# Optimization experiments

Hardware: AMD Instinct MI355X
Metric: run time of the kernel (lower is better)

## Reference

```python
import jax, jax.numpy as jnp
import numpy as np

H, W = 64, 64
DELTA = 5.0
EPS = 1e-8
ITERS = 3
LN_EPS = 1e-5


def _make_grid():
    # abs_grid in [-1, 1], shape (H, W, 2) -- matches S_p init range
    ys = jnp.linspace(-1.0, 1.0, H)
    xs = jnp.linspace(-1.0, 1.0, W)
    gy, gx = jnp.meshgrid(ys, xs, indexing='ij')
    return jnp.stack([gy, gx], axis=-1).astype(jnp.float32)


def _ln(x, g, b):
    m = jnp.mean(x, -1, keepdims=True)
    v = jnp.mean((x - m) ** 2, -1, keepdims=True)
    return (x - m) * jax.lax.rsqrt(v + LN_EPS) * g + b


def _mlp2(x, w1, b1, w2, b2):
    return jax.nn.relu(x @ w1.T + b1) @ w2.T + b2


def _gru(x, h, wih, whh, bih, bhh):
    gi = x @ wih.T + bih
    gh = h @ whh.T + bhh
    ir, iz, inn = jnp.split(gi, 3, -1)
    hr, hz, hn = jnp.split(gh, 3, -1)
    r = jax.nn.sigmoid(ir + hr)
    z = jax.nn.sigmoid(iz + hz)
    nn_ = jnp.tanh(inn + r * hn)
    return (1.0 - z) * nn_ + z * h


def setup_inputs() -> dict:
    key = jax.random.key(0)
    ks = jax.random.split(key, 30)
    b, n_s, d, hd = 8, 8, 128, 128
    n = H * W
    s = 0.02
    inp = {}
    inp['inputs'] = jax.random.normal(ks[0], (b, n, d), jnp.float32)
    inp['slots_init'] = jax.random.normal(ks[1], (b, n_s, d), jnp.float32)
    inp['S_p0'] = 2.0 * jax.random.uniform(ks[2], (b, n_s, 2), jnp.float32) - 1.0
    inp['S_s'] = 0.01 * jax.random.normal(ks[3], (b, n_s, 2), jnp.float32) + 0.1
    inp['S_r'] = (np.pi / 4.0) * jnp.tanh(jax.random.normal(ks[4], (b, n_s, 2, 2), jnp.float32))
    inp['Wq'] = s * jax.random.normal(ks[5], (d, d), jnp.float32)
    inp['Wk'] = s * jax.random.normal(ks[6], (d, d), jnp.float32)
    inp['Wv'] = s * jax.random.normal(ks[7], (d, d), jnp.float32)
    inp['g_w'] = s * jax.random.normal(ks[8], (d, 2), jnp.float32)
    inp['g_b'] = s * jax.random.normal(ks[9], (d,), jnp.float32)
    inp['f_w1'] = s * jax.random.normal(ks[10], (hd, d), jnp.float32)
    inp['f_b1'] = s * jax.random.normal(ks[11], (hd,), jnp.float32)
    inp['f_w2'] = s * jax.random.normal(ks[12], (d, hd), jnp.float32)
    inp['f_b2'] = s * jax.random.normal(ks[13], (d,), jnp.float32)
    inp['gru_wih'] = s * jax.random.normal(ks[14], (3 * d, d), jnp.float32)
    inp['gru_whh'] = s * jax.random.normal(ks[15], (3 * d, d), jnp.float32)
    inp['gru_bih'] = s * jax.random.normal(ks[16], (3 * d,), jnp.float32)
    inp['gru_bhh'] = s * jax.random.normal(ks[17], (3 * d,), jnp.float32)
    inp['mlp_w1'] = s * jax.random.normal(ks[18], (hd, d), jnp.float32)
    inp['mlp_b1'] = s * jax.random.normal(ks[19], (hd,), jnp.float32)
    inp['mlp_w2'] = s * jax.random.normal(ks[20], (d, hd), jnp.float32)
    inp['mlp_b2'] = s * jax.random.normal(ks[21], (d,), jnp.float32)
    inp['ln_s_g'] = jnp.ones((d,), jnp.float32)
    inp['ln_s_b'] = jnp.zeros((d,), jnp.float32)
    inp['ln_pf_g'] = jnp.ones((d,), jnp.float32)
    inp['ln_pf_b'] = jnp.zeros((d,), jnp.float32)
    return inp


def reference(inputs, slots_init, S_p0, S_s, S_r, Wq, Wk, Wv, g_w, g_b,
              f_w1, f_b1, f_w2, f_b2, gru_wih, gru_whh, gru_bih, gru_bhh,
              mlp_w1, mlp_b1, mlp_w2, mlp_b2, ln_s_g, ln_s_b, ln_pf_g, ln_pf_b):
    b, n, d = inputs.shape
    n_s = slots_init.shape[1]
    scale = d ** -0.5
    grid = _make_grid()            # (H, W, 2)
    grid_flat = grid.reshape(n, 2)  # (HW, 2)

    to_k = (inputs @ Wk.T)[:, None]  # (b, 1, n, d)
    to_v = (inputs @ Wv.T)[:, None]

    slots = slots_init
    S_p = S_p0
    for _ in range(ITERS):
        slots_prev = slots
        slots_n = _ln(slots, ln_s_g, ln_s_b)
        # per-slot relative grid: (b, n_s, H, W, 2)
        rel = (grid[None, None] - S_p[:, :, None, None, :]) / DELTA
        pos = (rel @ g_w.T + g_b).reshape(b, n_s, n, d)  # (b, n_s, HW, d)
        k = _mlp2(to_k + pos, f_w1, f_b1, f_w2, f_b2)     # (b, n_s, HW, d)
        v = _mlp2(to_v + pos, f_w1, f_b1, f_w2, f_b2)
        q = slots_n @ Wq.T                                # (b, n_s, d)
        dots = jnp.einsum('bid,bijd->bij', q, k) * scale  # (b, n_s, HW)
        attn = jax.nn.softmax(dots, axis=1) + EPS          # softmax over slots
        attn = attn / jnp.sum(attn, -1, keepdims=True)
        updates = jnp.einsum('bijd,bij->bid', v, attn)    # (b, n_s, d)
        # per-slot attention-weighted centroid (vectorized over slots)
        S_p = jnp.einsum('bij,jc->bic', attn, grid_flat) / jnp.sum(attn, -1, keepdims=True)
        slots = _gru(updates.reshape(-1, d), slots_prev.reshape(-1, d),
                     gru_wih, gru_whh, gru_bih, gru_bhh).reshape(b, n_s, d)
        slots = slots + _mlp2(_ln(slots, ln_pf_g, ln_pf_b), mlp_w1, mlp_b1, mlp_w2, mlp_b2)
    return slots, S_p, S_r, S_s
```

## Files before the change

kernel.cpp:

```cpp
#include <hip/hip_runtime.h>
#include <cstdint>
#include <cstddef>

#define SCALE  0.08838834764831845f
#define EPS_   1e-8f
#define LN_EPS_ 1e-5f

typedef unsigned short ushort_t;
typedef unsigned int uint_t;
typedef __attribute__((ext_vector_type(8))) short short8;
typedef __attribute__((ext_vector_type(4))) float f32x4;

constexpr int OFF_GFD   = 0;
constexpr int OFF_CB    = 256;
constexpr int OFF_QB    = 384;
constexpr int OFF_SP    = 448;
constexpr int OFF_OQ    = 576;
constexpr int OFF_SLOTS = 16960;
constexpr int OFF_ZP    = 25152;
constexpr int OFF_PP    = 29248;
constexpr int OFF_UP    = 37440;
constexpr int OFF_WKB   = 561728;
constexpr int OFF_WVB   = 569920;
constexpr int OFF_FW2T  = 578112;
constexpr int OFF_BKT   = 594496;
constexpr int OFF_BV    = 2691648;
constexpr int OFF_AB    = 4788800;

__device__ __forceinline__ float waveReduceSum(float v) {
#pragma unroll
  for (int m = 1; m < 64; m <<= 1) v += __shfl_xor(v, m, 64);
  return v;
}
__device__ __forceinline__ float bf2f(uint_t u) { return __uint_as_float(u << 16); }
__device__ __forceinline__ ushort_t f2bf(float f) {
  uint_t u = __float_as_uint(f);
  return (ushort_t)((u + 0x7fffu + ((u >> 16) & 1u)) >> 16);
}

__device__ __forceinline__ float halfDot(const float* __restrict__ Wrow,
                                         const float* xv, int h) {
  const float4* wr = (const float4*)Wrow + h * 16;
  const float4* xr = (const float4*)xv + h * 16;
  float4 a = {0.f, 0.f, 0.f, 0.f};
#pragma unroll
  for (int i = 0; i < 16; ++i) {
    float4 wv = wr[i], xq = xr[i];
    a.x = fmaf(wv.x, xq.x, a.x);
    a.y = fmaf(wv.y, xq.y, a.y);
    a.z = fmaf(wv.z, xq.z, a.z);
    a.w = fmaf(wv.w, xq.w, a.w);
  }
  return (a.x + a.y) + (a.z + a.w);
}

__device__ __forceinline__ float quarterDot(const float* __restrict__ Wrow,
                                            const float* xv, int h) {
  const float4* wr = (const float4*)Wrow + h * 8;
  const float4* xr = (const float4*)xv + h * 8;
  float4 a = {0.f, 0.f, 0.f, 0.f};
#pragma unroll
  for (int i = 0; i < 8; ++i) {
    float4 wv = wr[i], xq = xr[i];
    a.x = fmaf(wv.x, xq.x, a.x);
    a.y = fmaf(wv.y, xq.y, a.y);
    a.z = fmaf(wv.z, xq.z, a.z);
    a.w = fmaf(wv.w, xq.w, a.w);
  }
  return (a.x + a.y) + (a.z + a.w);
}
__device__ __forceinline__ float quadSum(float v) {
  v += __shfl_xor(v, 1, 64);
  v += __shfl_xor(v, 2, 64);
  return v;
}

__global__ __launch_bounds__(256) void kFold(
    const float* __restrict__ f_w1, const float* __restrict__ Wk,
    const float* __restrict__ Wv, const float* __restrict__ g_w,
    const float* __restrict__ g_b, const float* __restrict__ f_b1,
    const float* __restrict__ f_w2, const float* __restrict__ slots_init,
    const float* __restrict__ S_p0, const float* __restrict__ inputs,
    float* __restrict__ ws) {
  int blk = blockIdx.x, tid = threadIdx.x;
  if (blk < 128) {
    int isV = blk >> 6;
    int idx = (blk & 63) * 256 + tid;
    int h = idx >> 7, e = idx & 127;
    const float* Wm = isV ? Wv : Wk;
    float a = 0.f;
#pragma unroll 4
    for (int d = 0; d < 128; ++d) a = fmaf(f_w1[h * 128 + d], Wm[d * 128 + e], a);
    ((ushort_t*)(ws + (isV ? OFF_WVB : OFF_WKB)))[idx] = f2bf(a);
  } else if (blk == 128) {
    int h = tid >> 1, c = tid & 1;
    float a = 0.f;
    for (int d = 0; d < 128; ++d) a = fmaf(f_w1[h * 128 + d], g_w[d * 2 + c], a);
    ws[OFF_GFD + tid] = a * 0.2f;
  } else if (blk == 129) {
    if (tid < 128) {
      float a = f_b1[tid];
      for (int d = 0; d < 128; ++d) a = fmaf(f_w1[tid * 128 + d], g_b[d], a);
      ws[OFF_CB + tid] = a;
    }
  } else if (blk == 130) {
    for (int i = tid; i < 16384; i += 256)
      ws[OFF_FW2T + (i & 127) * 128 + (i >> 7)] = f_w2[i];
  } else if (blk < 135) {
    int base = (blk - 131) * 2048 + tid * 8;
    float4 a = *(const float4*)&slots_init[base];
    float4 b = *(const float4*)&slots_init[base + 4];
    *(float4*)&ws[OFF_SLOTS + base] = a;
    *(float4*)&ws[OFF_SLOTS + base + 4] = b;
  } else if (blk == 135) {
    if (tid < 128) ws[OFF_SP + tid] = S_p0[tid];
  } else {
    int idx = (blk - 136) * 256 + tid;
    const float4* src = (const float4*)(inputs + (size_t)idx * 8);
    float4 a = src[0], b = src[1];
    uint_t p0 = (uint_t)f2bf(a.x) | ((uint_t)f2bf(a.y) << 16);
    uint_t p1 = (uint_t)f2bf(a.z) | ((uint_t)f2bf(a.w) << 16);
    uint_t p2 = (uint_t)f2bf(b.x) | ((uint_t)f2bf(b.y) << 16);
    uint_t p3 = (uint_t)f2bf(b.z) | ((uint_t)f2bf(b.w) << 16);
    ((uint4*)((ushort_t*)(ws + OFF_AB)))[idx] = make_uint4(p0, p1, p2, p3);
  }
}

struct QSm { float yl[128]; float ql[128]; float red[4]; float red2[4]; };

__device__ void doQ(int bs, const float* __restrict__ Wq,
                    const float* __restrict__ f_b2,
                    const float* __restrict__ lnsg,
                    const float* __restrict__ lnsb,
                    float* __restrict__ ws, QSm& S) {
  int t = threadIdx.x, w = t >> 6, lane = t & 63;
  int d = w * 32 + (lane >> 1), h = lane & 1;
  const float* FW2T = ws + OFF_FW2T;
  float x = ws[OFF_SLOTS + bs * 128 + d];
  float m1 = waveReduceSum(h == 0 ? x : 0.f);
  float m2 = waveReduceSum(h == 0 ? x * x : 0.f);
  if (lane == 0) { S.red[w] = m1; S.red2[w] = m2; }
  __syncthreads();
  float mean = (S.red[0] + S.red[1] + S.red[2] + S.red[3]) * (1.f / 128.f);
  float var = (S.red2[0] + S.red2[1] + S.red2[2] + S.red2[3]) * (1.f / 128.f) - mean * mean;
  if (h == 0) S.yl[d] = (x - mean) * rsqrtf(var + LN_EPS_) * lnsg[d] + lnsb[d];
  __syncthreads();
  float q = halfDot(Wq + (size_t)d * 128, S.yl, h);
  q += __shfl_xor(q, 1, 64);
  if (h == 0) S.ql[d] = q;
  __syncthreads();
  float qv = waveReduceSum(h == 0 ? q * f_b2[d] : 0.f);
  if (lane == 0) S.red[w] = qv;
  float qf = halfDot(FW2T + (size_t)d * 128, S.ql, h);
  qf += __shfl_xor(qf, 1, 64);
  __syncthreads();
  if (t == 0) ws[OFF_QB + bs] = (S.red[0] + S.red[1] + S.red[2] + S.red[3]) * SCALE;
  if (h == 0) {
    float sp0 = ws[OFF_SP + bs * 2 + 0], sp1 = ws[OFF_SP + bs * 2 + 1];
    float offd = -(sp0 * ws[OFF_GFD + d * 2 + 0] + sp1 * ws[OFF_GFD + d * 2 + 1]);
    ws[OFF_OQ + (bs * 128 + d) * 2 + 0] = offd;
    ws[OFF_OQ + (bs * 128 + d) * 2 + 1] = qf * SCALE;
  }
}

__global__ __launch_bounds__(256) void kBaseQ(const float* __restrict__ Wq,
                                              const float* __restrict__ f_b2,
                                              const float* __restrict__ lnsg,
                                              const float* __restrict__ lnsb,
                                              float* __restrict__ ws) {
  __shared__ __align__(16) char smem[17408];
  int blk = blockIdx.x;
  if (blk >= 1024) {
    doQ(blk - 1024, Wq, f_b2, lnsg, lnsb, ws, *reinterpret_cast<QSm*>(smem));
    return;
  }
  char* ep = smem;
  const ushort_t* ab = (const ushort_t*)(ws + OFF_AB);
  int tid = threadIdx.x, w = tid >> 6, l = tid & 63;
  int lr = l & 15, lg = l >> 4;
  int mat = blk >> 9;
  int rb = blk & 511;
  int b = rb >> 6;
  int n0 = (rb & 63) * 64;
  const ushort_t* Wg = (const ushort_t*)(ws + (mat ? OFF_WVB : OFF_WKB));

  short8 afrag[4];
#pragma unroll
  for (int ks = 0; ks < 4; ++ks) {
    size_t row = (size_t)b * 4096 + n0 + w * 16 + lr;
    afrag[ks] = *(const short8*)(ab + row * 128 + ks * 32 + lg * 8);
  }
  float gf0a[8], gf1a[8], cba[8];
#pragma unroll
  for (int ct = 0; ct < 8; ++ct) {
    int c = ct * 16 + lr;
    gf0a[ct] = ws[OFF_GFD + c * 2 + 0];
    gf1a[ct] = ws[OFF_GFD + c * 2 + 1];
    cba[ct]  = ws[OFF_CB + c];
  }
  f32x4 acc[8];
#pragma unroll
  for (int ct = 0; ct < 8; ++ct) acc[ct] = (f32x4){0.f, 0.f, 0.f, 0.f};
#pragma unroll 2
  for (int ct = 0; ct < 8; ++ct) {
    short8 bfr[4];
#pragma unroll
    for (int ks = 0; ks < 4; ++ks)
      bfr[ks] = *(const short8*)(Wg + (ct * 16 + lr) * 128 + ks * 32 + lg * 8);
#pragma unroll
    for (int ks = 0; ks < 4; ++ks)
      acc[ct] = __builtin_amdgcn_mfma_f32_16x16x32_bf16(afrag[ks], bfr[ks], acc[ct], 0, 0, 0);
  }
#pragma unroll
  for (int ct = 0; ct < 8; ++ct) {
    int c = ct * 16 + lr;
    ushort_t pk[4];
#pragma unroll
    for (int r = 0; r < 4; ++r) {
      int nl = w * 16 + lg * 4 + r;
      int n = n0 + nl;
      float gy = -1.f + (float)(n >> 6) * (2.f / 63.f);
      float gx = -1.f + (float)(n & 63) * (2.f / 63.f);
      float o = acc[ct][r] + gy * gf0a[ct] + gx * gf1a[ct] + cba[ct];
      pk[r] = f2bf(o);
    }
    if (mat == 0) {
      int nl0 = w * 16 + lg * 4;
      int byte = (c * 128 + nl0 * 2) ^ ((c & 7) << 4);
      *(uint2*)(ep + byte) = make_uint2(
          (uint_t)pk[0] | ((uint_t)pk[1] << 16),
          (uint_t)pk[2] | ((uint_t)pk[3] << 16));
    } else {
      int nl0 = w * 16 + lg * 4;
#pragma unroll
      for (int r = 0; r < 4; ++r)
        *(ushort_t*)(ep + (nl0 + r) * 272 + c * 2) = pk[r];
    }
  }
  __syncthreads();
  if (mat == 0) {
    uint_t* outK = (uint_t*)(ws + OFF_BKT);
    for (int idx = tid; idx < 1024; idx += 256) {
      int dp = idx >> 4, j = idx & 15;
      int c0 = 2 * dp, c1 = 2 * dp + 1;
      uint2 aA = *(const uint2*)(ep + ((c0 * 128 + j * 8) ^ ((c0 & 7) << 4)));
      uint2 bA = *(const uint2*)(ep + ((c1 * 128 + j * 8) ^ ((c1 & 7) << 4)));
      uint4 o;
      o.x = (aA.x & 0xffffu) | (bA.x << 16);
      o.y = (aA.x >> 16) | (bA.x & 0xffff0000u);
      o.z = (aA.y & 0xffffu) | (bA.y << 16);
      o.w = (aA.y >> 16) | (bA.y & 0xffff0000u);
      *(uint4*)(outK + ((size_t)(b * 64 + dp)) * 4096 + n0 + j * 4) = o;
    }
  } else {
    ushort_t* outV = (ushort_t*)(ws + OFF_BV);
    for (int idx = tid; idx < 1024; idx += 256) {
      int nl = idx >> 4, j = idx & 15;
      uint4 v = *(const uint4*)(ep + nl * 272 + j * 16);
      *(uint4*)(outV + ((size_t)rb * 64 + nl) * 128 + j * 8) = v;
    }
  }
}

__global__ __launch_bounds__(256) void kAttn(float* __restrict__ ws) {
  __shared__ __align__(16) float OFFl[8][128];
  __shared__ __align__(16) float QFl[8][128];
  __shared__ float tp[64][37];
  __shared__ __align__(16) float al[64][12];
  __shared__ float Ush[4][8][132];
  int b = blockIdx.x >> 6, chunk = blockIdx.x & 63;
  int tid = threadIdx.x, w = tid >> 6, lane = tid & 63;
  int sb = b * 8;
  for (int f = tid; f < 1024; f += 256) {
    int s = f >> 7, d = f & 127;
    float2 oq = *(const float2*)&ws[OFF_OQ + ((sb + s) * 128 + d) * 2];
    OFFl[s][d] = oq.x;
    QFl[s][d] = oq.y;
  }
  float qbl[8];
#pragma unroll
  for (int s = 0; s < 8; ++s) qbl[s] = ws[OFF_QB + sb + s];
  __syncthreads();

  int n = chunk * 64 + lane;
  const uint_t* kpp = (const uint_t*)(ws + OFF_BKT) +
                      (size_t)b * 262144 + (size_t)(w * 16) * 4096 + n;
  float t[8];
#pragma unroll
  for (int s = 0; s < 8; ++s) t[s] = 0.f;
#pragma unroll 4
  for (int dp = 0; dp < 16; ++dp) {
    uint_t v = kpp[(size_t)dp * 4096];
    float k0 = bf2f(v & 0xffffu);
    float k1 = bf2f(v >> 16);
    int d0 = w * 32 + 2 * dp;
#pragma unroll
    for (int s = 0; s < 8; ++s) {
      float2 ofp = *(const float2*)&OFFl[s][d0];
      float2 qfp = *(const float2*)&QFl[s][d0];
      t[s] = fmaf(fmaxf(k0 + ofp.x, 0.f), qfp.x, t[s]);
      t[s] = fmaf(fmaxf(k1 + ofp.y, 0.f), qfp.y, t[s]);
    }
  }
#pragma unroll
  for (int s = 0; s < 8; ++s) tp[lane][s * 4 + w] = t[s];
  __syncthreads();
  float a[8], den = 0.f;
#pragma unroll
  for (int s = 0; s < 8; ++s)
    t[s] = tp[lane][s * 4 + 0] + tp[lane][s * 4 + 1] +
           tp[lane][s * 4 + 2] + tp[lane][s * 4 + 3] + qbl[s];
  float mx = t[0];
#pragma unroll
  for (int s = 1; s < 8; ++s) mx = fmaxf(mx, t[s]);
#pragma unroll
  for (int s = 0; s < 8; ++s) { a[s] = __expf(t[s] - mx); den += a[s]; }
  float inv = 1.0f / den;
#pragma unroll
  for (int s = 0; s < 8; ++s) a[s] = fmaf(a[s], inv, EPS_);
  if (w == 0) {
    float gy = -1.f + (float)(n >> 6) * (2.f / 63.f);
    float gx = -1.f + (float)(n & 63) * (2.f / 63.f);
#pragma unroll
    for (int s = 0; s < 8; ++s) al[lane][s] = a[s];
#pragma unroll
    for (int s = 0; s < 8; ++s) {
      float z = waveReduceSum(a[s]);
      float p0 = waveReduceSum(a[s] * gy);
      float p1 = waveReduceSum(a[s] * gx);
      if (lane == 0) {
        ws[OFF_ZP + (b * 64 + chunk) * 8 + s] = z;
        ws[OFF_PP + ((b * 64 + chunk) * 8 + s) * 2 + 0] = p0;
        ws[OFF_PP + ((b * 64 + chunk) * 8 + s) * 2 + 1] = p1;
      }
    }
  }
  __syncthreads();

  int c0 = 2 * lane;
  float offv0[8], offv1[8];
#pragma unroll
  for (int s = 0; s < 8; ++s) {
    float2 of2 = *(const float2*)&OFFl[s][c0];
    offv0[s] = of2.x;
    offv1[s] = of2.y;
  }
  float Ua0[8], Ua1[8];
#pragma unroll
  for (int s = 0; s < 8; ++s) { Ua0[s] = 0.f; Ua1[s] = 0.f; }
  const ushort_t* vp = (const ushort_t*)(ws + OFF_BV) +
                       ((size_t)(b * 4096 + chunk * 64 + w * 16)) * 128 + c0;
#pragma unroll 4
  for (int i = 0; i < 16; ++i) {
    uint_t vraw = *(const uint_t*)(vp + (size_t)i * 128);
    float v0 = bf2f(vraw & 0xffffu);
    float v1 = bf2f(vraw >> 16);
    int ii = w * 16 + i;
    float4 a0 = *(const float4*)&al[ii][0];
    float4 a1 = *(const float4*)&al[ii][4];
    float asv[8] = {a0.x, a0.y, a0.z, a0.w, a1.x, a1.y, a1.z, a1.w};
#pragma unroll
    for (int s = 0; s < 8; ++s) {
      Ua0[s] = fmaf(asv[s], fmaxf(v0 + offv0[s], 0.f), Ua0[s]);
      Ua1[s] = fmaf(asv[s], fmaxf(v1 + offv1[s], 0.f), Ua1[s]);
    }
  }
#pragma unroll
  for (int s = 0; s < 8; ++s) {
    Ush[w][s][c0] = Ua0[s];
    Ush[w][s][c0 + 1] = Ua1[s];
  }
  __syncthreads();
  for (int f = tid; f < 1024; f += 256) {
    int s = f >> 7, c = f & 127;
    float v = Ush[0][s][c] + Ush[1][s][c] + Ush[2][s][c] + Ush[3][s][c];
    ws[OFF_UP + ((size_t)(b * 64 + chunk) * 8 + s) * 128 + c] = v;
  }
}

__global__ __launch_bounds__(512) void kCQ(
    const float* __restrict__ Wq, const float* __restrict__ f_w2,
    const float* __restrict__ f_b2, const float* __restrict__ wih,
    const float* __restrict__ whh, const float* __restrict__ bih,
    const float* __restrict__ bhh, const float* __restrict__ mw1,
    const float* __restrict__ mb1, const float* __restrict__ mw2,
    const float* __restrict__ mb2, const float* __restrict__ lnpg,
    const float* __restrict__ lnpb, const float* __restrict__ lnsg,
    const float* __restrict__ lnsb, const float* __restrict__ S_r,
    const float* __restrict__ S_s, float* __restrict__ ws,
    float* __restrict__ out, int last) {
  int bs = blockIdx.x;
  int t = threadIdx.x;
  if (bs == 64) {
    if (t < 256) out[8320 + t] = S_r[t];
    else if (t < 384) out[8576 + t - 256] = S_s[t - 256];
    return;
  }
  int b = bs >> 3, s = bs & 7;
  int w = t >> 6, lane = t & 63;
  int d = t >> 2, h = t & 3;
  __shared__ __align__(16) float ul[128], xl[128], sl[128], yl[128], hml[128];
  __shared__ float red[8], red2[8];
  const float* FW2T = ws + OFF_FW2T;
  float zv = ws[OFF_ZP + (b * 64 + lane) * 8 + s];
  float2 pv = *(const float2*)&ws[OFF_PP + ((size_t)(b * 64 + lane) * 8 + s) * 2];
  float Z = waveReduceSum(zv);
  float P0 = waveReduceSum(pv.x);
  float P1 = waveReduceSum(pv.y);
  float invZ = 1.f / Z, sp0 = P0 * invZ, sp1 = P1 * invZ;
  float u = 0.f;
  const float* up = ws + OFF_UP + ((size_t)(b * 64 + h * 16) * 8 + s) * 128 + d;
#pragma unroll
  for (int ch = 0; ch < 16; ++ch) u += up[(size_t)ch * 1024];
  u = quadSum(u);
  if (h == 0) { ul[d] = u * invZ; sl[d] = ws[OFF_SLOTS + bs * 128 + d]; }
  if (t == 0) {
    ws[OFF_SP + bs * 2 + 0] = sp0;
    ws[OFF_SP + bs * 2 + 1] = sp1;
    if (last) {
      out[8192 + bs * 2 + 0] = sp0;
      out[8192 + bs * 2 + 1] = sp1;
    }
  }
  __syncthreads();
  float xa = quadSum(quarterDot(f_w2 + (size_t)d * 128, ul, h));
  if (h == 0) xl[d] = xa + f_b2[d];
  __syncthreads();
  float ir = quarterDot(wih + (size_t)d * 128, xl, h);
  float iz = quarterDot(wih + (size_t)(128 + d) * 128, xl, h);
  float in_ = quarterDot(wih + (size_t)(256 + d) * 128, xl, h);
  float hr = quarterDot(whh + (size_t)d * 128, sl, h);
  float hz = quarterDot(whh + (size_t)(128 + d) * 128, sl, h);
  float hn = quarterDot(whh + (size_t)(256 + d) * 128, sl, h);
  ir = quadSum(ir); iz = quadSum(iz); in_ = quadSum(in_);
  hr = quadSum(hr); hz = quadSum(hz); hn = quadSum(hn);
  float hnew = 0.f;
  if (h == 0) {
    float rg = 1.f / (1.f + __expf(-(ir + bih[d] + hr + bhh[d])));
    float zg = 1.f / (1.f + __expf(-(iz + bih[128 + d] + hz + bhh[128 + d])));
    float ng = tanhf(in_ + bih[256 + d] + rg * (hn + bhh[256 + d]));
    hnew = (1.f - zg) * ng + zg * sl[d];
  }
  float m1 = waveReduceSum(h == 0 ? hnew : 0.f);
  float m2 = waveReduceSum(h == 0 ? hnew * hnew : 0.f);
  if (lane == 0) { red[w] = m1; red2[w] = m2; }
  __syncthreads();
  float mean = 0.f, var = 0.f;
#pragma unroll
  for (int i = 0; i < 8; ++i) { mean += red[i]; var += red2[i]; }
  mean *= (1.f / 128.f);
  var = var * (1.f / 128.f) - mean * mean;
  if (h == 0) yl[d] = (hnew - mean) * rsqrtf(var + LN_EPS_) * lnpg[d] + lnpb[d];
  __syncthreads();
  float hm = quadSum(quarterDot(mw1 + (size_t)d * 128, yl, h));
  if (h == 0) hml[d] = fmaxf(hm + mb1[d], 0.f);
  __syncthreads();
  float oa = quadSum(quarterDot(mw2 + (size_t)d * 128, hml, h));
  float o = 0.f;
  if (h == 0) {
    o = hnew + mb2[d] + oa;
    ws[OFF_SLOTS + bs * 128 + d] = o;
    if (last) out[bs * 128 + d] = o;
  }
  float n1 = waveReduceSum(h == 0 ? o : 0.f);
  float n2 = waveReduceSum(h == 0 ? o * o : 0.f);
  if (lane == 0) { red[w] = n1; red2[w] = n2; }
  __syncthreads();
  float mean2 = 0.f, var2 = 0.f;
#pragma unroll
  for (int i = 0; i < 8; ++i) { mean2 += red[i]; var2 += red2[i]; }
  mean2 *= (1.f / 128.f);
  var2 = var2 * (1.f / 128.f) - mean2 * mean2;
  if (h == 0) yl[d] = (o - mean2) * rsqrtf(var2 + LN_EPS_) * lnsg[d] + lnsb[d];
  __syncthreads();
  float q = quadSum(quarterDot(Wq + (size_t)d * 128, yl, h));
  if (h == 0) xl[d] = q;
  __syncthreads();
  float qv = waveReduceSum(h == 0 ? q * f_b2[d] : 0.f);
  if (lane == 0) red[w] = qv;
  float qf = quadSum(quarterDot(FW2T + (size_t)d * 128, xl, h));
  __syncthreads();
  if (t == 0) {
    float qb = 0.f;
#pragma unroll
    for (int i = 0; i < 8; ++i) qb += red[i];
    ws[OFF_QB + bs] = qb * SCALE;
  }
  if (h == 0) {
    float offd = -(sp0 * ws[OFF_GFD + d * 2 + 0] + sp1 * ws[OFF_GFD + d * 2 + 1]);
    ws[OFF_OQ + (bs * 128 + d) * 2 + 0] = offd;
    ws[OFF_OQ + (bs * 128 + d) * 2 + 1] = qf * SCALE;
  }
}

extern "C" void kernel_launch(void* const* d_in, const int* in_sizes, int n_in,
                              void* d_out, int out_size, void* d_ws, size_t ws_size,
                              hipStream_t stream) {
  const float* inputs     = (const float*)d_in[0];
  const float* slots_init = (const float*)d_in[1];
  const float* S_p0       = (const float*)d_in[2];
  const float* S_s        = (const float*)d_in[3];
  const float* S_r        = (const float*)d_in[4];
  const float* Wq   = (const float*)d_in[5];
  const float* Wk   = (const float*)d_in[6];
  const float* Wv   = (const float*)d_in[7];
  const float* g_w  = (const float*)d_in[8];
  const float* g_b  = (const float*)d_in[9];
  const float* f_w1 = (const float*)d_in[10];
  const float* f_b1 = (const float*)d_in[11];
  const float* f_w2 = (const float*)d_in[12];
  const float* f_b2 = (const float*)d_in[13];
  const float* gwih = (const float*)d_in[14];
  const float* gwhh = (const float*)d_in[15];
  const float* gbih = (const float*)d_in[16];
  const float* gbhh = (const float*)d_in[17];
  const float* mw1  = (const float*)d_in[18];
  const float* mb1  = (const float*)d_in[19];
  const float* mw2  = (const float*)d_in[20];
  const float* mb2  = (const float*)d_in[21];
  const float* lnsg = (const float*)d_in[22];
  const float* lnsb = (const float*)d_in[23];
  const float* lnpg = (const float*)d_in[24];
  const float* lnpb = (const float*)d_in[25];
  float* ws  = (float*)d_ws;
  float* out = (float*)d_out;

  kFold<<<392, 256, 0, stream>>>(f_w1, Wk, Wv, g_w, g_b, f_b1, f_w2,
                                 slots_init, S_p0, inputs, ws);
  kBaseQ<<<1088, 256, 0, stream>>>(Wq, f_b2, lnsg, lnsb, ws);
  for (int it = 0; it < 3; ++it) {
    int last = (it == 2);
    kAttn<<<512, 256, 0, stream>>>(ws);
    kCQ<<<64 + last, 512, 0, stream>>>(Wq, f_w2, f_b2, gwih, gwhh, gbih, gbhh,
                                       mw1, mb1, mw2, mb2, lnpg, lnpb,
                                       lnsg, lnsb, S_r, S_s, ws, out, last);
  }
}
```

Measured before the change: 165.6 us.

## Fuse K/V projection with first attention pass and fold initial Q into prep kernel

```diff
diff --git a/kernel.cpp b/kernel.cpp
--- a/kernel.cpp
+++ b/kernel.cpp
@@ -81,7 +81,10 @@
     const float* __restrict__ g_b, const float* __restrict__ f_b1,
     const float* __restrict__ f_w2, const float* __restrict__ slots_init,
     const float* __restrict__ S_p0, const float* __restrict__ inputs,
-    float* __restrict__ ws) {
+    const float* __restrict__ Wq, const float* __restrict__ f_b2,
+    const float* __restrict__ lnsg, const float* __restrict__ lnsb,
+    const float* __restrict__ S_r, const float* __restrict__ S_s,
+    float* __restrict__ ws, float* __restrict__ out) {
   int blk = blockIdx.x, tid = threadIdx.x;
   if (blk < 128) {
     int isV = blk >> 6;
@@ -114,7 +117,7 @@
     *(float4*)&ws[OFF_SLOTS + base + 4] = b;
   } else if (blk == 135) {
     if (tid < 128) ws[OFF_SP + tid] = S_p0[tid];
-  } else {
+  } else if (blk < 392) {
     int idx = (blk - 136) * 256 + tid;
     const float4* src = (const float4*)(inputs + (size_t)idx * 8);
     float4 a = src[0], b = src[1];
@@ -123,159 +126,70 @@
     uint_t p2 = (uint_t)f2bf(b.x) | ((uint_t)f2bf(b.y) << 16);
     uint_t p3 = (uint_t)f2bf(b.z) | ((uint_t)f2bf(b.w) << 16);
     ((uint4*)((ushort_t*)(ws + OFF_AB)))[idx] = make_uint4(p0, p1, p2, p3);
-  }
-}
-
-struct QSm { float yl[128]; float ql[128]; float red[4]; float red2[4]; };
-
-__device__ void doQ(int bs, const float* __restrict__ Wq,
-                    const float* __restrict__ f_b2,
-                    const float* __restrict__ lnsg,
-                    const float* __restrict__ lnsb,
-                    float* __restrict__ ws, QSm& S) {
-  int t = threadIdx.x, w = t >> 6, lane = t & 63;
-  int d = w * 32 + (lane >> 1), h = lane & 1;
-  const float* FW2T = ws + OFF_FW2T;
-  float x = ws[OFF_SLOTS + bs * 128 + d];
-  float m1 = waveReduceSum(h == 0 ? x : 0.f);
-  float m2 = waveReduceSum(h == 0 ? x * x : 0.f);
-  if (lane == 0) { S.red[w] = m1; S.red2[w] = m2; }
-  __syncthreads();
-  float mean = (S.red[0] + S.red[1] + S.red[2] + S.red[3]) * (1.f / 128.f);
-  float var = (S.red2[0] + S.red2[1] + S.red2[2] + S.red2[3]) * (1.f / 128.f) - mean * mean;
-  if (h == 0) S.yl[d] = (x - mean) * rsqrtf(var + LN_EPS_) * lnsg[d] + lnsb[d];
-  __syncthreads();
-  float q = halfDot(Wq + (size_t)d * 128, S.yl, h);
-  q += __shfl_xor(q, 1, 64);
-  if (h == 0) S.ql[d] = q;
-  __syncthreads();
-  float qv = waveReduceSum(h == 0 ? q * f_b2[d] : 0.f);
-  if (lane == 0) S.red[w] = qv;
-  float qf = halfDot(FW2T + (size_t)d * 128, S.ql, h);
-  qf += __shfl_xor(qf, 1, 64);
-  __syncthreads();
-  if (t == 0) ws[OFF_QB + bs] = (S.red[0] + S.red[1] + S.red[2] + S.red[3]) * SCALE;
-  if (h == 0) {
-    float sp0 = ws[OFF_SP + bs * 2 + 0], sp1 = ws[OFF_SP + bs * 2 + 1];
-    float offd = -(sp0 * ws[OFF_GFD + d * 2 + 0] + sp1 * ws[OFF_GFD + d * 2 + 1]);
-    ws[OFF_OQ + (bs * 128 + d) * 2 + 0] = offd;
-    ws[OFF_OQ + (bs * 128 + d) * 2 + 1] = qf * SCALE;
-  }
-}
-
-__global__ __launch_bounds__(256) void kBaseQ(const float* __restrict__ Wq,
-                                              const float* __restrict__ f_b2,
-                                              const float* __restrict__ lnsg,
-                                              const float* __restrict__ lnsb,
-                                              float* __restrict__ ws) {
-  __shared__ __align__(16) char smem[17408];
-  int blk = blockIdx.x;
-  if (blk >= 1024) {
-    doQ(blk - 1024, Wq, f_b2, lnsg, lnsb, ws, *reinterpret_cast<QSm*>(smem));
-    return;
-  }
-  char* ep = smem;
-  const ushort_t* ab = (const ushort_t*)(ws + OFF_AB);
-  int tid = threadIdx.x, w = tid >> 6, l = tid & 63;
-  int lr = l & 15, lg = l >> 4;
-  int mat = blk >> 9;
-  int rb = blk & 511;
-  int b = rb >> 6;
-  int n0 = (rb & 63) * 64;
-  const ushort_t* Wg = (const ushort_t*)(ws + (mat ? OFF_WVB : OFF_WKB));
-
-  short8 afrag[4];
-#pragma unroll
-  for (int ks = 0; ks < 4; ++ks) {
-    size_t row = (size_t)b * 4096 + n0 + w * 16 + lr;
-    afrag[ks] = *(const short8*)(ab + row * 128 + ks * 32 + lg * 8);
-  }
-  float gf0a[8], gf1a[8], cba[8];
-#pragma unroll
-  for (int ct = 0; ct < 8; ++ct) {
-    int c = ct * 16 + lr;
-    gf0a[ct] = ws[OFF_GFD + c * 2 + 0];
-    gf1a[ct] = ws[OFF_GFD + c * 2 + 1];
-    cba[ct]  = ws[OFF_CB + c];
-  }
-  f32x4 acc[8];
-#pragma unroll
-  for (int ct = 0; ct < 8; ++ct) acc[ct] = (f32x4){0.f, 0.f, 0.f, 0.f};
-#pragma unroll 2
-  for (int ct = 0; ct < 8; ++ct) {
-    short8 bfr[4];
-#pragma unroll
-    for (int ks = 0; ks < 4; ++ks)
-      bfr[ks] = *(const short8*)(Wg + (ct * 16 + lr) * 128 + ks * 32 + lg * 8);
-#pragma unroll
-    for (int ks = 0; ks < 4; ++ks)
-      acc[ct] = __builtin_amdgcn_mfma_f32_16x16x32_bf16(afrag[ks], bfr[ks], acc[ct], 0, 0, 0);
-  }
-#pragma unroll
-  for (int ct = 0; ct < 8; ++ct) {
-    int c = ct * 16 + lr;
-    ushort_t pk[4];
-#pragma unroll
-    for (int r = 0; r < 4; ++r) {
-      int nl = w * 16 + lg * 4 + r;
-      int n = n0 + nl;
-      float gy = -1.f + (float)(n >> 6) * (2.f / 63.f);
-      float gx = -1.f + (float)(n & 63) * (2.f / 63.f);
-      float o = acc[ct][r] + gy * gf0a[ct] + gx * gf1a[ct] + cba[ct];
-      pk[r] = f2bf(o);
-    }
-    if (mat == 0) {
-      int nl0 = w * 16 + lg * 4;
-      int byte = (c * 128 + nl0 * 2) ^ ((c & 7) << 4);
-      *(uint2*)(ep + byte) = make_uint2(
-          (uint_t)pk[0] | ((uint_t)pk[1] << 16),
-          (uint_t)pk[2] | ((uint_t)pk[3] << 16));
-    } else {
-      int nl0 = w * 16 + lg * 4;
-#pragma unroll
-      for (int r = 0; r < 4; ++r)
-        *(ushort_t*)(ep + (nl0 + r) * 272 + c * 2) = pk[r];
-    }
-  }
-  __syncthreads();
-  if (mat == 0) {
-    uint_t* outK = (uint_t*)(ws + OFF_BKT);
-    for (int idx = tid; idx < 1024; idx += 256) {
-      int dp = idx >> 4, j = idx & 15;
-      int c0 = 2 * dp, c1 = 2 * dp + 1;
-      uint2 aA = *(const uint2*)(ep + ((c0 * 128 + j * 8) ^ ((c0 & 7) << 4)));
-      uint2 bA = *(const uint2*)(ep + ((c1 * 128 + j * 8) ^ ((c1 & 7) << 4)));
-      uint4 o;
-      o.x = (aA.x & 0xffffu) | (bA.x << 16);
-      o.y = (aA.x >> 16) | (bA.x & 0xffff0000u);
-      o.z = (aA.y & 0xffffu) | (bA.y << 16);
-      o.w = (aA.y >> 16) | (bA.y & 0xffff0000u);
-      *(uint4*)(outK + ((size_t)(b * 64 + dp)) * 4096 + n0 + j * 4) = o;
+  } else if (blk < 456) {
+    int bs = blk - 392;
+    __shared__ __align__(16) float yl[128], ql[128], gwsp[128];
+    __shared__ float red[4], red2[4];
+    int t = tid, w = t >> 6, lane = t & 63;
+    int d = w * 32 + (lane >> 1), h = lane & 1;
+    float sp0 = S_p0[bs * 2 + 0], sp1 = S_p0[bs * 2 + 1];
+    if (t < 128) gwsp[t] = sp0 * g_w[t * 2 + 0] + sp1 * g_w[t * 2 + 1];
+    float x = slots_init[bs * 128 + d];
+    float m1 = waveReduceSum(h == 0 ? x : 0.f);
+    float m2 = waveReduceSum(h == 0 ? x * x : 0.f);
+    if (lane == 0) { red[w] = m1; red2[w] = m2; }
+    __syncthreads();
+    float mean = (red[0] + red[1] + red[2] + red[3]) * (1.f / 128.f);
+    float var = (red2[0] + red2[1] + red2[2] + red2[3]) * (1.f / 128.f) - mean * mean;
+    if (h == 0) yl[d] = (x - mean) * rsqrtf(var + LN_EPS_) * lnsg[d] + lnsb[d];
+    __syncthreads();
+    float q = halfDot(Wq + (size_t)d * 128, yl, h);
+    q += __shfl_xor(q, 1, 64);
+    if (h == 0) ql[d] = q;
+    __syncthreads();
+    float qv = waveReduceSum(h == 0 ? q * f_b2[d] : 0.f);
+    if (lane == 0) red[w] = qv;
+    float qf = 0.f;
+    const float* fcol = f_w2 + (size_t)(h * 64) * 128 + d;
+#pragma unroll 4
+    for (int e = 0; e < 64; ++e) qf = fmaf(ql[h * 64 + e], fcol[(size_t)e * 128], qf);
+    qf += __shfl_xor(qf, 1, 64);
+    float od = halfDot(f_w1 + (size_t)d * 128, gwsp, h);
+    od += __shfl_xor(od, 1, 64);
+    __syncthreads();
+    if (t == 0) ws[OFF_QB + bs] = (red[0] + red[1] + red[2] + red[3]) * SCALE;
+    if (h == 0) {
+      ws[OFF_OQ + (bs * 128 + d) * 2 + 0] = -0.2f * od;
+      ws[OFF_OQ + (bs * 128 + d) * 2 + 1] = qf * SCALE;
     }
   } else {
-    ushort_t* outV = (ushort_t*)(ws + OFF_BV);
-    for (int idx = tid; idx < 1024; idx += 256) {
-      int nl = idx >> 4, j = idx & 15;
-      uint4 v = *(const uint4*)(ep + nl * 272 + j * 16);
-      *(uint4*)(outV + ((size_t)rb * 64 + nl) * 128 + j * 8) = v;
-    }
-  }
-}
-
-__global__ __launch_bounds__(256) void kAttn(float* __restrict__ ws) {
-  __shared__ __align__(16) float OFFl[8][128];
-  __shared__ __align__(16) float QFl[8][128];
-  __shared__ float tp[64][37];
-  __shared__ __align__(16) float al[64][12];
-  __shared__ float Ush[4][8][132];
-  int b = blockIdx.x >> 6, chunk = blockIdx.x & 63;
+    out[8320 + tid] = S_r[tid];
+    if (tid < 128) out[8576 + tid] = S_s[tid];
+  }
+}
+
+struct AtSm {
+  float OFFl[8][128];
+  float QFl[8][128];
+  float tp[64][37];
+  float al[64][12];
+  float Ush[4][8][132];
+};
+
+__device__ void doAttn(int b, int chunk, float* __restrict__ ws, AtSm& S) {
   int tid = threadIdx.x, w = tid >> 6, lane = tid & 63;
   int sb = b * 8;
+  int c0 = 2 * lane;
+  const ushort_t* vp = (const ushort_t*)(ws + OFF_BV) +
+                       ((size_t)(b * 4096 + chunk * 64 + w * 16)) * 128 + c0;
+  uint_t varr[16];
+#pragma unroll
+  for (int i = 0; i < 16; ++i) varr[i] = *(const uint_t*)(vp + (size_t)i * 128);
   for (int f = tid; f < 1024; f += 256) {
     int s = f >> 7, d = f & 127;
     float2 oq = *(const float2*)&ws[OFF_OQ + ((sb + s) * 128 + d) * 2];
-    OFFl[s][d] = oq.x;
-    QFl[s][d] = oq.y;
+    S.OFFl[s][d] = oq.x;
+    S.QFl[s][d] = oq.y;
   }
   float qbl[8];
 #pragma unroll
@@ -296,20 +210,20 @@
     int d0 = w * 32 + 2 * dp;
 #pragma unroll
     for (int s = 0; s < 8; ++s) {
-      float2 ofp = *(const float2*)&OFFl[s][d0];
-      float2 qfp = *(const float2*)&QFl[s][d0];
+      float2 ofp = *(const float2*)&S.OFFl[s][d0];
+      float2 qfp = *(const float2*)&S.QFl[s][d0];
       t[s] = fmaf(fmaxf(k0 + ofp.x, 0.f), qfp.x, t[s]);
       t[s] = fmaf(fmaxf(k1 + ofp.y, 0.f), qfp.y, t[s]);
     }
   }
 #pragma unroll
-  for (int s = 0; s < 8; ++s) tp[lane][s * 4 + w] = t[s];
+  for (int s = 0; s < 8; ++s) S.tp[lane][s * 4 + w] = t[s];
   __syncthreads();
   float a[8], den = 0.f;
 #pragma unroll
   for (int s = 0; s < 8; ++s)
-    t[s] = tp[lane][s * 4 + 0] + tp[lane][s * 4 + 1] +
-           tp[lane][s * 4 + 2] + tp[lane][s * 4 + 3] + qbl[s];
+    t[s] = S.tp[lane][s * 4 + 0] + S.tp[lane][s * 4 + 1] +
+           S.tp[lane][s * 4 + 2] + S.tp[lane][s * 4 + 3] + qbl[s];
   float mx = t[0];
 #pragma unroll
   for (int s = 1; s < 8; ++s) mx = fmaxf(mx, t[s]);
@@ -322,7 +236,7 @@
     float gy = -1.f + (float)(n >> 6) * (2.f / 63.f);
     float gx = -1.f + (float)(n & 63) * (2.f / 63.f);
 #pragma unroll
-    for (int s = 0; s < 8; ++s) al[lane][s] = a[s];
+    for (int s = 0; s < 8; ++s) S.al[lane][s] = a[s];
 #pragma unroll
     for (int s = 0; s < 8; ++s) {
       float z = waveReduceSum(a[s]);
@@ -337,27 +251,24 @@
   }
   __syncthreads();
 
-  int c0 = 2 * lane;
   float offv0[8], offv1[8];
 #pragma unroll
   for (int s = 0; s < 8; ++s) {
-    float2 of2 = *(const float2*)&OFFl[s][c0];
+    float2 of2 = *(const float2*)&S.OFFl[s][c0];
     offv0[s] = of2.x;
     offv1[s] = of2.y;
   }
   float Ua0[8], Ua1[8];
 #pragma unroll
   for (int s = 0; s < 8; ++s) { Ua0[s] = 0.f; Ua1[s] = 0.f; }
-  const ushort_t* vp = (const ushort_t*)(ws + OFF_BV) +
-                       ((size_t)(b * 4096 + chunk * 64 + w * 16)) * 128 + c0;
 #pragma unroll 4
   for (int i = 0; i < 16; ++i) {
-    uint_t vraw = *(const uint_t*)(vp + (size_t)i * 128);
+    uint_t vraw = varr[i];
     float v0 = bf2f(vraw & 0xffffu);
     float v1 = bf2f(vraw >> 16);
     int ii = w * 16 + i;
-    float4 a0 = *(const float4*)&al[ii][0];
-    float4 a1 = *(const float4*)&al[ii][4];
+    float4 a0 = *(const float4*)&S.al[ii][0];
+    float4 a1 = *(const float4*)&S.al[ii][4];
     float asv[8] = {a0.x, a0.y, a0.z, a0.w, a1.x, a1.y, a1.z, a1.w};
 #pragma unroll
     for (int s = 0; s < 8; ++s) {
@@ -367,15 +278,118 @@
   }
 #pragma unroll
   for (int s = 0; s < 8; ++s) {
-    Ush[w][s][c0] = Ua0[s];
-    Ush[w][s][c0 + 1] = Ua1[s];
+    S.Ush[w][s][c0] = Ua0[s];
+    S.Ush[w][s][c0 + 1] = Ua1[s];
   }
   __syncthreads();
   for (int f = tid; f < 1024; f += 256) {
     int s = f >> 7, c = f & 127;
-    float v = Ush[0][s][c] + Ush[1][s][c] + Ush[2][s][c] + Ush[3][s][c];
+    float v = S.Ush[0][s][c] + S.Ush[1][s][c] + S.Ush[2][s][c] + S.Ush[3][s][c];
     ws[OFF_UP + ((size_t)(b * 64 + chunk) * 8 + s) * 128 + c] = v;
   }
+}
+
+union SmU {
+  char ep[17408];
+  AtSm at;
+};
+
+__global__ __launch_bounds__(256) void kBA(float* __restrict__ ws) {
+  __shared__ __align__(16) SmU S;
+  int blk = blockIdx.x;
+  int tid = threadIdx.x, w = tid >> 6, l = tid & 63;
+  int lr = l & 15, lg = l >> 4;
+  int b = blk >> 6, chunk = blk & 63;
+  int n0 = chunk * 64;
+  const ushort_t* ab = (const ushort_t*)(ws + OFF_AB);
+  char* ep = S.ep;
+
+  short8 afrag[4];
+#pragma unroll
+  for (int ks = 0; ks < 4; ++ks) {
+    size_t row = (size_t)b * 4096 + n0 + w * 16 + lr;
+    afrag[ks] = *(const short8*)(ab + row * 128 + ks * 32 + lg * 8);
+  }
+  float gf0a[8], gf1a[8], cba[8];
+#pragma unroll
+  for (int ct = 0; ct < 8; ++ct) {
+    int c = ct * 16 + lr;
+    gf0a[ct] = ws[OFF_GFD + c * 2 + 0];
+    gf1a[ct] = ws[OFF_GFD + c * 2 + 1];
+    cba[ct]  = ws[OFF_CB + c];
+  }
+  for (int mat = 0; mat < 2; ++mat) {
+    const ushort_t* Wg = (const ushort_t*)(ws + (mat ? OFF_WVB : OFF_WKB));
+    f32x4 acc[8];
+#pragma unroll
+    for (int ct = 0; ct < 8; ++ct) acc[ct] = (f32x4){0.f, 0.f, 0.f, 0.f};
+#pragma unroll 2
+    for (int ct = 0; ct < 8; ++ct) {
+      short8 bfr[4];
+#pragma unroll
+      for (int ks = 0; ks < 4; ++ks)
+        bfr[ks] = *(const short8*)(Wg + (ct * 16 + lr) * 128 + ks * 32 + lg * 8);
+#pragma unroll
+      for (int ks = 0; ks < 4; ++ks)
+        acc[ct] = __builtin_amdgcn_mfma_f32_16x16x32_bf16(afrag[ks], bfr[ks], acc[ct], 0, 0, 0);
+    }
+#pragma unroll
+    for (int ct = 0; ct < 8; ++ct) {
+      int c = ct * 16 + lr;
+      ushort_t pk[4];
+#pragma unroll
+      for (int r = 0; r < 4; ++r) {
+        int nl = w * 16 + lg * 4 + r;
+        int n = n0 + nl;
+        float gy = -1.f + (float)(n >> 6) * (2.f / 63.f);
+        float gx = -1.f + (float)(n & 63) * (2.f / 63.f);
+        float o = acc[ct][r] + gy * gf0a[ct] + gx * gf1a[ct] + cba[ct];
+        pk[r] = f2bf(o);
+      }
+      if (mat == 0) {
+        int nl0 = w * 16 + lg * 4;
+        int byte = (c * 128 + nl0 * 2) ^ ((c & 7) << 4);
+        *(uint2*)(ep + byte) = make_uint2(
+            (uint_t)pk[0] | ((uint_t)pk[1] << 16),
+            (uint_t)pk[2] | ((uint_t)pk[3] << 16));
+      } else {
+        int nl0 = w * 16 + lg * 4;
+#pragma unroll
+        for (int r = 0; r < 4; ++r)
+          *(ushort_t*)(ep + (nl0 + r) * 272 + c * 2) = pk[r];
+      }
+    }
+    __syncthreads();
+    if (mat == 0) {
+      uint_t* outK = (uint_t*)(ws + OFF_BKT);
+      for (int idx = tid; idx < 1024; idx += 256) {
+        int dp = idx >> 4, j = idx & 15;
+        int c0 = 2 * dp, c1 = 2 * dp + 1;
+        uint2 aA = *(const uint2*)(ep + ((c0 * 128 + j * 8) ^ ((c0 & 7) << 4)));
+        uint2 bA = *(const uint2*)(ep + ((c1 * 128 + j * 8) ^ ((c1 & 7) << 4)));
+        uint4 o;
+        o.x = (aA.x & 0xffffu) | (bA.x << 16);
+        o.y = (aA.x >> 16) | (bA.x & 0xffff0000u);
+        o.z = (aA.y & 0xffffu) | (bA.y << 16);
+        o.w = (aA.y >> 16) | (bA.y & 0xffff0000u);
+        *(uint4*)(outK + ((size_t)(b * 64 + dp)) * 4096 + n0 + j * 4) = o;
+      }
+    } else {
+      ushort_t* outV = (ushort_t*)(ws + OFF_BV);
+      for (int idx = tid; idx < 1024; idx += 256) {
+        int nl = idx >> 4, j = idx & 15;
+        uint4 v = *(const uint4*)(ep + nl * 272 + j * 16);
+        *(uint4*)(outV + ((size_t)(b * 4096 + n0 + nl)) * 128 + j * 8) = v;
+      }
+    }
+    __syncthreads();
+  }
+  doAttn(b, chunk, ws, S.at);
+}
+
+__global__ __launch_bounds__(256) void kAttn(float* __restrict__ ws) {
+  __shared__ __align__(16) AtSm S;
+  doAttn(blockIdx.x >> 6, blockIdx.x & 63, ws, S);
 }
 
 __global__ __launch_bounds__(512) void kCQ(
@@ -386,16 +400,10 @@
     const float* __restrict__ mb1, const float* __restrict__ mw2,
     const float* __restrict__ mb2, const float* __restrict__ lnpg,
     const float* __restrict__ lnpb, const float* __restrict__ lnsg,
-    const float* __restrict__ lnsb, const float* __restrict__ S_r,
-    const float* __restrict__ S_s, float* __restrict__ ws,
+    const float* __restrict__ lnsb, float* __restrict__ ws,
     float* __restrict__ out, int last) {
   int bs = blockIdx.x;
   int t = threadIdx.x;
-  if (bs == 64) {
-    if (t < 256) out[8320 + t] = S_r[t];
-    else if (t < 384) out[8576 + t - 256] = S_s[t - 256];
-    return;
-  }
   int b = bs >> 3, s = bs & 7;
   int w = t >> 6, lane = t & 63;
   int d = t >> 2, h = t & 3;
@@ -525,14 +533,15 @@
   float* ws  = (float*)d_ws;
   float* out = (float*)d_out;
 
-  kFold<<<392, 256, 0, stream>>>(f_w1, Wk, Wv, g_w, g_b, f_b1, f_w2,
-                                 slots_init, S_p0, inputs, ws);
-  kBaseQ<<<1088, 256, 0, stream>>>(Wq, f_b2, lnsg, lnsb, ws);
+  kFold<<<457, 256, 0, stream>>>(f_w1, Wk, Wv, g_w, g_b, f_b1, f_w2,
+                                 slots_init, S_p0, inputs, Wq, f_b2,
+                                 lnsg, lnsb, S_r, S_s, ws, out);
+  kBA<<<512, 256, 0, stream>>>(ws);
   for (int it = 0; it < 3; ++it) {
     int last = (it == 2);
-    kAttn<<<512, 256, 0, stream>>>(ws);
-    kCQ<<<64 + last, 512, 0, stream>>>(Wq, f_w2, f_b2, gwih, gwhh, gbih, gbhh,
-                                       mw1, mb1, mw2, mb2, lnpg, lnpb,
-                                       lnsg, lnsb, S_r, S_s, ws, out, last);
-  }
-}
+    kCQ<<<64, 512, 0, stream>>>(Wq, f_w2, f_b2, gwih, gwhh, gbih, gbhh,
+                                mw1, mb1, mw2, mb2, lnpg, lnpb,
+                                lnsg, lnsb, ws, out, last);
+    if (!last) kAttn<<<512, 256, 0, stream>>>(ws);
+  }
+}
```

Result: slower. 178.0 us (+7.5%).

## Halve kAttn chunk size to double block count and prefetch V early

Applied to the files above, without the earlier changes.

```diff
diff --git a/kernel.cpp b/kernel.cpp
--- a/kernel.cpp
+++ b/kernel.cpp
@@ -18,14 +18,14 @@
 constexpr int OFF_OQ    = 576;
 constexpr int OFF_SLOTS = 16960;
 constexpr int OFF_ZP    = 25152;
-constexpr int OFF_PP    = 29248;
-constexpr int OFF_UP    = 37440;
-constexpr int OFF_WKB   = 561728;
-constexpr int OFF_WVB   = 569920;
-constexpr int OFF_FW2T  = 578112;
-constexpr int OFF_BKT   = 594496;
-constexpr int OFF_BV    = 2691648;
-constexpr int OFF_AB    = 4788800;
+constexpr int OFF_PP    = 33344;
+constexpr int OFF_UP    = 49728;
+constexpr int OFF_WKB   = 1098304;
+constexpr int OFF_WVB   = 1106496;
+constexpr int OFF_FW2T  = 1114688;
+constexpr int OFF_BKT   = 1131072;
+constexpr int OFF_BV    = 3228224;
+constexpr int OFF_AB    = 5325376;
 
 __device__ __forceinline__ float waveReduceSum(float v) {
 #pragma unroll
@@ -265,12 +265,19 @@
 __global__ __launch_bounds__(256) void kAttn(float* __restrict__ ws) {
   __shared__ __align__(16) float OFFl[8][128];
   __shared__ __align__(16) float QFl[8][128];
-  __shared__ float tp[64][37];
-  __shared__ __align__(16) float al[64][12];
+  __shared__ float tp[32][33];
+  __shared__ __align__(16) float al[32][12];
   __shared__ float Ush[4][8][132];
-  int b = blockIdx.x >> 6, chunk = blockIdx.x & 63;
+  int b = blockIdx.x >> 7, chunk = blockIdx.x & 127;
   int tid = threadIdx.x, w = tid >> 6, lane = tid & 63;
   int sb = b * 8;
+  int n0 = chunk * 32;
+  int c0 = 2 * lane;
+  const ushort_t* vp = (const ushort_t*)(ws + OFF_BV) +
+                       ((size_t)(b * 4096 + n0 + w * 8)) * 128 + c0;
+  uint_t varr[8];
+#pragma unroll
+  for (int i = 0; i < 8; ++i) varr[i] = *(const uint_t*)(vp + (size_t)i * 128);
   for (int f = tid; f < 1024; f += 256) {
     int s = f >> 7, d = f & 127;
     float2 oq = *(const float2*)&ws[OFF_OQ + ((sb + s) * 128 + d) * 2];
@@ -282,18 +289,19 @@
   for (int s = 0; s < 8; ++s) qbl[s] = ws[OFF_QB + sb + s];
   __syncthreads();
 
-  int n = chunk * 64 + lane;
+  int p = lane >> 1, half = lane & 1;
+  int n = n0 + p;
   const uint_t* kpp = (const uint_t*)(ws + OFF_BKT) +
-                      (size_t)b * 262144 + (size_t)(w * 16) * 4096 + n;
+                      (size_t)b * 262144 + (size_t)(w * 16 + half * 8) * 4096 + n;
   float t[8];
 #pragma unroll
   for (int s = 0; s < 8; ++s) t[s] = 0.f;
-#pragma unroll 4
-  for (int dp = 0; dp < 16; ++dp) {
-    uint_t v = kpp[(size_t)dp * 4096];
+#pragma unroll
+  for (int j = 0; j < 8; ++j) {
+    uint_t v = kpp[(size_t)j * 4096];
     float k0 = bf2f(v & 0xffffu);
     float k1 = bf2f(v >> 16);
-    int d0 = w * 32 + 2 * dp;
+    int d0 = w * 32 + (half * 8 + j) * 2;
 #pragma unroll
     for (int s = 0; s < 8; ++s) {
       float2 ofp = *(const float2*)&OFFl[s][d0];
@@ -303,13 +311,17 @@
     }
   }
 #pragma unroll
-  for (int s = 0; s < 8; ++s) tp[lane][s * 4 + w] = t[s];
-  __syncthreads();
+  for (int s = 0; s < 8; ++s) {
+    t[s] += __shfl_xor(t[s], 1, 64);
+    if (half == 0) tp[p][s * 4 + w] = t[s];
+  }
+  __syncthreads();
+  int p2 = lane & 31;
   float a[8], den = 0.f;
 #pragma unroll
   for (int s = 0; s < 8; ++s)
-    t[s] = tp[lane][s * 4 + 0] + tp[lane][s * 4 + 1] +
-           tp[lane][s * 4 + 2] + tp[lane][s * 4 + 3] + qbl[s];
+    t[s] = tp[p2][s * 4 + 0] + tp[p2][s * 4 + 1] +
+           tp[p2][s * 4 + 2] + tp[p2][s * 4 + 3] + qbl[s];
   float mx = t[0];
 #pragma unroll
   for (int s = 1; s < 8; ++s) mx = fmaxf(mx, t[s]);
@@ -319,25 +331,28 @@
 #pragma unroll
   for (int s = 0; s < 8; ++s) a[s] = fmaf(a[s], inv, EPS_);
   if (w == 0) {
-    float gy = -1.f + (float)(n >> 6) * (2.f / 63.f);
-    float gx = -1.f + (float)(n & 63) * (2.f / 63.f);
-#pragma unroll
-    for (int s = 0; s < 8; ++s) al[lane][s] = a[s];
+    int n2 = n0 + p2;
+    float gy = -1.f + (float)(n2 >> 6) * (2.f / 63.f);
+    float gx = -1.f + (float)(n2 & 63) * (2.f / 63.f);
+    bool lo = (lane < 32);
+    if (lo) {
+#pragma unroll
+      for (int s = 0; s < 8; ++s) al[p2][s] = a[s];
+    }
 #pragma unroll
     for (int s = 0; s < 8; ++s) {
-      float z = waveReduceSum(a[s]);
-      float p0 = waveReduceSum(a[s] * gy);
-      float p1 = waveReduceSum(a[s] * gx);
+      float z = waveReduceSum(lo ? a[s] : 0.f);
+      float p0 = waveReduceSum(lo ? a[s] * gy : 0.f);
+      float p1 = waveReduceSum(lo ? a[s] * gx : 0.f);
       if (lane == 0) {
-        ws[OFF_ZP + (b * 64 + chunk) * 8 + s] = z;
-        ws[OFF_PP + ((b * 64 + chunk) * 8 + s) * 2 + 0] = p0;
-        ws[OFF_PP + ((b * 64 + chunk) * 8 + s) * 2 + 1] = p1;
+        ws[OFF_ZP + (b * 128 + chunk) * 8 + s] = z;
+        ws[OFF_PP + ((b * 128 + chunk) * 8 + s) * 2 + 0] = p0;
+        ws[OFF_PP + ((b * 128 + chunk) * 8 + s) * 2 + 1] = p1;
       }
     }
   }
   __syncthreads();
 
-  int c0 = 2 * lane;
   float offv0[8], offv1[8];
 #pragma unroll
   for (int s = 0; s < 8; ++s) {
@@ -348,14 +363,12 @@
   float Ua0[8], Ua1[8];
 #pragma unroll
   for (int s = 0; s < 8; ++s) { Ua0[s] = 0.f; Ua1[s] = 0.f; }
-  const ushort_t* vp = (const ushort_t*)(ws + OFF_BV) +
-                       ((size_t)(b * 4096 + chunk * 64 + w * 16)) * 128 + c0;
-#pragma unroll 4
-  for (int i = 0; i < 16; ++i) {
-    uint_t vraw = *(const uint_t*)(vp + (size_t)i * 128);
+#pragma unroll
+  for (int i = 0; i < 8; ++i) {
+    uint_t vraw = varr[i];
     float v0 = bf2f(vraw & 0xffffu);
     float v1 = bf2f(vraw >> 16);
-    int ii = w * 16 + i;
+    int ii = w * 8 + i;
     float4 a0 = *(const float4*)&al[ii][0];
     float4 a1 = *(const float4*)&al[ii][4];
     float asv[8] = {a0.x, a0.y, a0.z, a0.w, a1.x, a1.y, a1.z, a1.w};
@@ -374,7 +387,7 @@
   for (int f = tid; f < 1024; f += 256) {
     int s = f >> 7, c = f & 127;
     float v = Ush[0][s][c] + Ush[1][s][c] + Ush[2][s][c] + Ush[3][s][c];
-    ws[OFF_UP + ((size_t)(b * 64 + chunk) * 8 + s) * 128 + c] = v;
+    ws[OFF_UP + ((size_t)(b * 128 + chunk) * 8 + s) * 128 + c] = v;
   }
 }
 
@@ -402,16 +415,18 @@
   __shared__ __align__(16) float ul[128], xl[128], sl[128], yl[128], hml[128];
   __shared__ float red[8], red2[8];
   const float* FW2T = ws + OFF_FW2T;
-  float zv = ws[OFF_ZP + (b * 64 + lane) * 8 + s];
-  float2 pv = *(const float2*)&ws[OFF_PP + ((size_t)(b * 64 + lane) * 8 + s) * 2];
+  float zv = ws[OFF_ZP + (b * 128 + lane) * 8 + s] +
+             ws[OFF_ZP + (b * 128 + 64 + lane) * 8 + s];
+  float2 pva = *(const float2*)&ws[OFF_PP + ((size_t)((b * 128 + lane) * 8 + s)) * 2];
+  float2 pvb = *(const float2*)&ws[OFF_PP + ((size_t)((b * 128 + 64 + lane) * 8 + s)) * 2];
   float Z = waveReduceSum(zv);
-  float P0 = waveReduceSum(pv.x);
-  float P1 = waveReduceSum(pv.y);
+  float P0 = waveReduceSum(pva.x + pvb.x);
+  float P1 = waveReduceSum(pva.y + pvb.y);
   float invZ = 1.f / Z, sp0 = P0 * invZ, sp1 = P1 * invZ;
   float u = 0.f;
-  const float* up = ws + OFF_UP + ((size_t)(b * 64 + h * 16) * 8 + s) * 128 + d;
-#pragma unroll
-  for (int ch = 0; ch < 16; ++ch) u += up[(size_t)ch * 1024];
+  const float* up = ws + OFF_UP + ((size_t)(b * 128 + h * 32) * 8 + s) * 128 + d;
+#pragma unroll
+  for (int ch = 0; ch < 32; ++ch) u += up[(size_t)ch * 1024];
   u = quadSum(u);
   if (h == 0) { ul[d] = u * invZ; sl[d] = ws[OFF_SLOTS + bs * 128 + d]; }
   if (t == 0) {
@@ -530,7 +545,7 @@
   kBaseQ<<<1088, 256, 0, stream>>>(Wq, f_b2, lnsg, lnsb, ws);
   for (int it = 0; it < 3; ++it) {
     int last = (it == 2);
-    kAttn<<<512, 256, 0, stream>>>(ws);
+    kAttn<<<1024, 256, 0, stream>>>(ws);
     kCQ<<<64 + last, 512, 0, stream>>>(Wq, f_w2, f_b2, gwih, gwhh, gbih, gbhh,
                                        mw1, mb1, mw2, mb2, lnpg, lnpb,
                                        lnsg, lnsb, S_r, S_s, ws, out, last);
```

Result: slower. 213.4 us (+28.9%).
